# Optimization experiments

Hardware: AMD Instinct MI355X
Metric: run time of the kernel (lower is better)

Reference implementation:

```python
import jax, jax.numpy as jnp
import numpy as np
import math

DM, DP, P = 1024, 128, 256
B, S = 8, 4096

def setup_inputs() -> dict:
    key = jax.random.key(0)
    ks = jax.random.split(key, 7)
    sd = lambda fan_in: 1.0 / math.sqrt(fan_in)
    return {
        "x": jax.random.normal(ks[0], (B, S, DM), jnp.float32),
        "prim_embeds": jax.random.normal(ks[1], (P, DP), jnp.float32),
        "Wq": jax.random.normal(ks[2], (DP, DM), jnp.float32) * sd(DM),
        "Wk": jax.random.normal(ks[3], (DP, DP), jnp.float32) * sd(DP),
        "Wv": jax.random.normal(ks[4], (DP, DP), jnp.float32) * sd(DP),
        "Wo": jax.random.normal(ks[5], (DM, DP), jnp.float32) * sd(DP),
        "gate_w": jax.random.normal(ks[6], (1, DM), jnp.float32) * sd(DM),
        "gate_b": jnp.zeros((1,), jnp.float32),
    }

def reference(x, prim_embeds, Wq, Wk, Wv, Wo, gate_w, gate_b):
    # q: [B,S,dp]; k,v: [P,dp]
    q = jnp.einsum('bsm,pm->bsp', x, Wq)          # p here = d_prim
    k = prim_embeds @ Wk.T                         # [P, dp]
    v = prim_embeds @ Wv.T                         # [P, dp]
    scale = 1.0 / math.sqrt(q.shape[-1])
    scores = jnp.einsum('bsd,pd->bsp', q, k) * scale  # [B,S,P]
    attn = jax.nn.softmax(scores, axis=-1)
    ctx = jnp.einsum('bsp,pd->bsd', attn, v)       # [B,S,dp]
    out = jnp.einsum('bsd,md->bsm', ctx, Wo)       # [B,S,dm]
    gate = jax.nn.sigmoid(jnp.einsum('bsm,om->bso', x, gate_w) + gate_b)  # [B,S,1]
    return gate * out
```

## Files before the change

kernel.cpp:

```cpp
#include <hip/hip_runtime.h>
#include <hip/hip_bf16.h>

typedef unsigned short ushort_t;
typedef __attribute__((ext_vector_type(8))) short short8;
typedef __attribute__((ext_vector_type(8))) unsigned short ushort8;
typedef __attribute__((ext_vector_type(4))) float f32x4;

#define MFMA16(a,b,c) __builtin_amdgcn_mfma_f32_16x16x32_bf16((a),(b),(c),0,0,0)

__device__ __forceinline__ ushort_t f2bf(float f) {
  unsigned int u = __builtin_bit_cast(unsigned int, f);
  u += 0x7FFFu + ((u >> 16) & 1u);
  return (ushort_t)(u >> 16);
}
__device__ __forceinline__ unsigned int pack2bf(float a, float b) {
  unsigned int ua = __builtin_bit_cast(unsigned int, a);
  unsigned int ub = __builtin_bit_cast(unsigned int, b);
  ua += 0x7FFFu + ((ua >> 16) & 1u);
  ub += 0x7FFFu + ((ub >> 16) & 1u);
  return (ua >> 16) | (ub & 0xFFFF0000u);
}

#define DMd 1024
#define DPd 128
#define PPd 256

#define KWQ_OFF 0
#define KWQ_SIZE (8*17*4*512)
#define VWO_OFF KWQ_SIZE
#define VWO_SIZE (64*8*512)
#define KV_BYTE_OFF ((size_t)(KWQ_SIZE + VWO_SIZE) * 2)

__global__ __launch_bounds__(256) void prep1_kernel(
    const float* __restrict__ prim, const float* __restrict__ Wk,
    const float* __restrict__ Wv, ushort_t* __restrict__ ws) {
  __shared__ __align__(16) float Wl[128 * 132];
  __shared__ __align__(16) float pl[2 * 128];
  const int t = threadIdx.x;
  const int mat = blockIdx.x & 1;
  const int p0 = (blockIdx.x >> 1) * 2;
  const float* W = mat ? Wv : Wk;
  #pragma unroll
  for (int i = 0; i < 16; ++i) {
    int w = (i * 256 + t) * 4;
    int row = w >> 7, col = w & 127;
    *(float4*)&Wl[row * 132 + col] = *(const float4*)(W + w);
  }
  if (t < 64) {
    int row = t >> 5, col = (t & 31) * 4;
    *(float4*)&pl[row * 128 + col] = *(const float4*)(prim + (p0 + row) * 128 + col);
  }
  __syncthreads();
  const int d = t & 127, slot = t >> 7;
  float a0 = 0.f, a1 = 0.f, a2 = 0.f, a3 = 0.f;
  #pragma unroll
  for (int j = 0; j < 128; j += 4) {
    float4 w4 = *(const float4*)&Wl[d * 132 + j];
    float4 p4 = *(const float4*)&pl[slot * 128 + j];
    a0 += w4.x * p4.x; a1 += w4.y * p4.y; a2 += w4.z * p4.z; a3 += w4.w * p4.w;
  }
  float r = (a0 + a1) + (a2 + a3);
  float* kf = (float*)((char*)ws + KV_BYTE_OFF);
  float* vT = kf + 32768;
  if (mat == 0) kf[(p0 + slot) * 128 + d] = r;
  else          vT[d * 256 + p0 + slot] = r;
}

__global__ __launch_bounds__(256) void prep2_kernel(
    const float* __restrict__ Wq, const float* __restrict__ Wo,
    const float* __restrict__ gate_w, ushort_t* __restrict__ ws) {
  const float* kf = (const float*)((const char*)ws + KV_BYTE_OFF);
  const float* vT = kf + 32768;
  __shared__ __align__(16) float tile[8 * 128];
  const int b = blockIdx.x, t = threadIdx.x;
  float acc[8];
  #pragma unroll
  for (int j = 0; j < 8; ++j) acc[j] = 0.f;
  if (b < 136) {
    const int pt = b >> 2, ms = b & 3;
    const int p0 = pt * 8;
    const int p  = p0 + (t >> 5);
    const int m0 = ms * 256 + (t & 31) * 8;
    if (p0 < 256) {
      *(float4*)&tile[t * 4] = *(const float4*)(kf + p0 * 128 + t * 4);
      __syncthreads();
      const float* kp = &tile[(t >> 5) * 128];
      for (int d = 0; d < 128; d += 4) {
        float4 kv = *(const float4*)&kp[d];
        float4 qa0 = *(const float4*)(Wq + (d + 0) * 1024 + m0);
        float4 qb0 = *(const float4*)(Wq + (d + 0) * 1024 + m0 + 4);
        float4 qa1 = *(const float4*)(Wq + (d + 1) * 1024 + m0);
        float4 qb1 = *(const float4*)(Wq + (d + 1) * 1024 + m0 + 4);
        float4 qa2 = *(const float4*)(Wq + (d + 2) * 1024 + m0);
        float4 qb2 = *(const float4*)(Wq + (d + 2) * 1024 + m0 + 4);
        float4 qa3 = *(const float4*)(Wq + (d + 3) * 1024 + m0);
        float4 qb3 = *(const float4*)(Wq + (d + 3) * 1024 + m0 + 4);
        acc[0] += kv.x*qa0.x + kv.y*qa1.x + kv.z*qa2.x + kv.w*qa3.x;
        acc[1] += kv.x*qa0.y + kv.y*qa1.y + kv.z*qa2.y + kv.w*qa3.y;
        acc[2] += kv.x*qa0.z + kv.y*qa1.z + kv.z*qa2.z + kv.w*qa3.z;
        acc[3] += kv.x*qa0.w + kv.y*qa1.w + kv.z*qa2.w + kv.w*qa3.w;
        acc[4] += kv.x*qb0.x + kv.y*qb1.x + kv.z*qb2.x + kv.w*qb3.x;
        acc[5] += kv.x*qb0.y + kv.y*qb1.y + kv.z*qb2.y + kv.w*qb3.y;
        acc[6] += kv.x*qb0.z + kv.y*qb1.z + kv.z*qb2.z + kv.w*qb3.z;
        acc[7] += kv.x*qb0.w + kv.y*qb1.w + kv.z*qb2.w + kv.w*qb3.w;
      }
    } else if (p == 256) {
      #pragma unroll
      for (int j = 0; j < 8; ++j) acc[j] = gate_w[m0 + j];
    }
    const int c = m0 >> 7, ct = p >> 4, k4 = (m0 >> 5) & 3;
    const int row = ((m0 >> 3) & 3) * 16 + (p & 15);
    ushort8 u;
    #pragma unroll
    for (int j = 0; j < 8; ++j) u[j] = f2bf(acc[j]);
    *(ushort8*)&ws[KWQ_OFF + ((size_t)(c * 17 + ct) * 4 + k4) * 512 + (size_t)row * 8] = u;
  } else {
    const int mb  = b - 136;
    const int m0t = mb * 8;
    const int m   = m0t + (t >> 5);
    const int p8  = (t & 31) * 8;
    *(float4*)&tile[t * 4] = *(const float4*)(Wo + (size_t)m0t * 128 + t * 4);
    __syncthreads();
    const float* wo = &tile[(t >> 5) * 128];
    for (int d = 0; d < 128; d += 4) {
      float4 wv = *(const float4*)&wo[d];
      float4 va0 = *(const float4*)(vT + (d + 0) * 256 + p8);
      float4 vb0 = *(const float4*)(vT + (d + 0) * 256 + p8 + 4);
      float4 va1 = *(const float4*)(vT + (d + 1) * 256 + p8);
      float4 vb1 = *(const float4*)(vT + (d + 1) * 256 + p8 + 4);
      float4 va2 = *(const float4*)(vT + (d + 2) * 256 + p8);
      float4 vb2 = *(const float4*)(vT + (d + 2) * 256 + p8 + 4);
      float4 va3 = *(const float4*)(vT + (d + 3) * 256 + p8);
      float4 vb3 = *(const float4*)(vT + (d + 3) * 256 + p8 + 4);
      acc[0] += wv.x*va0.x + wv.y*va1.x + wv.z*va2.x + wv.w*va3.x;
      acc[1] += wv.x*va0.y + wv.y*va1.y + wv.z*va2.y + wv.w*va3.y;
      acc[2] += wv.x*va0.z + wv.y*va1.z + wv.z*va2.z + wv.w*va3.z;
      acc[3] += wv.x*va0.w + wv.y*va1.w + wv.z*va2.w + wv.w*va3.w;
      acc[4] += wv.x*vb0.x + wv.y*vb1.x + wv.z*vb2.x + wv.w*vb3.x;
      acc[5] += wv.x*vb0.y + wv.y*vb1.y + wv.z*vb2.y + wv.w*vb3.y;
      acc[6] += wv.x*vb0.z + wv.y*vb1.z + wv.z*vb2.z + wv.w*vb3.z;
      acc[7] += wv.x*vb0.w + wv.y*vb1.w + wv.z*vb2.w + wv.w*vb3.w;
    }
    const int ctg = m >> 4, k8 = p8 >> 5;
    const int row = ((p8 >> 3) & 3) * 16 + (m & 15);
    ushort8 u;
    #pragma unroll
    for (int j = 0; j < 8; ++j) u[j] = f2bf(acc[j]);
    *(ushort8*)&ws[VWO_OFF + ((size_t)(ctg * 8 + k8) * 512) + (size_t)row * 8] = u;
  }
}

#define LDX 136
#define LDSLAB 264

__global__ __launch_bounds__(256, 2) void fused_kernel(
    const float* __restrict__ x, const float* __restrict__ gate_b,
    const ushort_t* __restrict__ ws, float* __restrict__ out)
{
  __shared__ __align__(16) char smem[2 * 32 * LDX * 2 + 32 * 4 * 4 * 2 + 32 * 4];
  ushort_t* xt0      = (ushort_t*)smem;
  ushort_t* xt1      = xt0 + 32 * LDX;
  ushort_t* slab     = (ushort_t*)smem;
  float*    pmax     = (float*)(smem + 2 * 32 * LDX * 2);
  float*    psum     = pmax + 128;
  float*    gate_lds = psum + 128;

  const int t = threadIdx.x, wid = t >> 6, lane = t & 63;
  const int quad = lane >> 4, l16 = lane & 15;
  const int tok0 = blockIdx.x * 32;

  f32x4 acc[2][5];
  #pragma unroll
  for (int rt = 0; rt < 2; ++rt)
    #pragma unroll
    for (int ctl = 0; ctl < 5; ++ctl) acc[rt][ctl] = (f32x4){0.f,0.f,0.f,0.f};

  #pragma unroll
  for (int i = 0; i < 4; ++i) {
    int flat = i * 1024 + t * 4;
    int row = flat >> 7, col = flat & 127;
    float4 fv = *(const float4*)(x + (size_t)(tok0 + row) * 1024 + col);
    unsigned int pk0 = pack2bf(fv.x, fv.y), pk1 = pack2bf(fv.z, fv.w);
    *(unsigned long long*)&xt0[row * LDX + col] =
        (unsigned long long)pk0 | ((unsigned long long)pk1 << 32);
  }
  __syncthreads();

  for (int c = 0; c < 8; ++c) {
    ushort_t* cur = (c & 1) ? xt1 : xt0;
    ushort_t* nxt = (c & 1) ? xt0 : xt1;
    float4 fv[4];
    if (c < 7) {
      #pragma unroll
      for (int i = 0; i < 4; ++i) {
        int flat = i * 1024 + t * 4;
        int row = flat >> 7, col = flat & 127;
        fv[i] = *(const float4*)(x + (size_t)(tok0 + row) * 1024 + (c + 1) * 128 + col);
      }
    }
    #pragma unroll
    for (int k4 = 0; k4 < 4; ++k4) {
      short8 a[2];
      #pragma unroll
      for (int rt = 0; rt < 2; ++rt)
        a[rt] = *(const short8*)&cur[(rt * 16 + l16) * LDX + k4 * 32 + quad * 8];
      #pragma unroll
      for (int ctl = 0; ctl < 5; ++ctl) {
        if (ctl == 4 && wid != 3) continue;
        const int ct = wid * 4 + ctl;
        short8 bfr = *(const short8*)&ws[KWQ_OFF +
            ((size_t)(c * 17 + ct) * 4 + k4) * 512 + (size_t)lane * 8];
        #pragma unroll
        for (int rt = 0; rt < 2; ++rt) acc[rt][ctl] = MFMA16(a[rt], bfr, acc[rt][ctl]);
      }
    }
    if (c < 7) {
      #pragma unroll
      for (int i = 0; i < 4; ++i) {
        int flat = i * 1024 + t * 4;
        int row = flat >> 7, col = flat & 127;
        unsigned int pk0 = pack2bf(fv[i].x, fv[i].y), pk1 = pack2bf(fv[i].z, fv[i].w);
        *(unsigned long long*)&nxt[row * LDX + col] =
            (unsigned long long)pk0 | ((unsigned long long)pk1 << 32);
      }
      __syncthreads();
    }
  }

  const float SC = 0.08838834764831845f * 1.44269504088896f;
  float Mx[2][4];
  #pragma unroll
  for (int rt = 0; rt < 2; ++rt)
    #pragma unroll
    for (int r = 0; r < 4; ++r) {
      float m = acc[rt][0][r];
      #pragma unroll
      for (int ctl = 1; ctl < 4; ++ctl) m = fmaxf(m, acc[rt][ctl][r]);
      #pragma unroll
      for (int msk = 1; msk < 16; msk <<= 1) m = fmaxf(m, __shfl_xor(m, msk, 64));
      Mx[rt][r] = m;
    }
  if (l16 == 0) {
    #pragma unroll
    for (int rt = 0; rt < 2; ++rt)
      #pragma unroll
      for (int r = 0; r < 4; ++r)
        pmax[(rt * 16 + quad * 4 + r) * 4 + wid] = Mx[rt][r];
  }
  __syncthreads();
  float Mf[2][4];
  #pragma unroll
  for (int rt = 0; rt < 2; ++rt)
    #pragma unroll
    for (int r = 0; r < 4; ++r) {
      f32x4 pm = *(f32x4*)&pmax[(rt * 16 + quad * 4 + r) * 4];
      Mf[rt][r] = fmaxf(fmaxf(pm[0], pm[1]), fmaxf(pm[2], pm[3]));
    }
  float Sm[2][4];
  #pragma unroll
  for (int rt = 0; rt < 2; ++rt)
    #pragma unroll
    for (int r = 0; r < 4; ++r) Sm[rt][r] = 0.f;
  #pragma unroll
  for (int rt = 0; rt < 2; ++rt)
    #pragma unroll
    for (int ctl = 0; ctl < 4; ++ctl)
      #pragma unroll
      for (int r = 0; r < 4; ++r) {
        float e = exp2f((acc[rt][ctl][r] - Mf[rt][r]) * SC);
        acc[rt][ctl][r] = e;
        Sm[rt][r] += e;
      }
  #pragma unroll
  for (int rt = 0; rt < 2; ++rt)
    #pragma unroll
    for (int r = 0; r < 4; ++r) {
      #pragma unroll
      for (int msk = 1; msk < 16; msk <<= 1) Sm[rt][r] += __shfl_xor(Sm[rt][r], msk, 64);
    }
  if (l16 == 0) {
    #pragma unroll
    for (int rt = 0; rt < 2; ++rt)
      #pragma unroll
      for (int r = 0; r < 4; ++r)
        psum[(rt * 16 + quad * 4 + r) * 4 + wid] = Sm[rt][r];
    if (wid == 3) {
      float gb = gate_b[0];
      #pragma unroll
      for (int rt = 0; rt < 2; ++rt)
        #pragma unroll
        for (int r = 0; r < 4; ++r) {
          float lg = acc[rt][4][r] + gb;
          gate_lds[rt * 16 + quad * 4 + r] = 1.f / (1.f + __expf(-lg));
        }
    }
  }
  __syncthreads();
  float scl[2][4];
  #pragma unroll
  for (int rt = 0; rt < 2; ++rt)
    #pragma unroll
    for (int r = 0; r < 4; ++r) {
      f32x4 ps = *(f32x4*)&psum[(rt * 16 + quad * 4 + r) * 4];
      float g = gate_lds[rt * 16 + quad * 4 + r];
      scl[rt][r] = g / (ps[0] + ps[1] + ps[2] + ps[3]);
    }

  #pragma unroll
  for (int rt = 0; rt < 2; ++rt)
    #pragma unroll
    for (int ctl = 0; ctl < 4; ++ctl)
      #pragma unroll
      for (int r = 0; r < 4; ++r)
        slab[(rt * 16 + quad * 4 + r) * LDSLAB + (wid * 4 + ctl) * 16 + l16] =
            f2bf(acc[rt][ctl][r] * scl[rt][r]);
  __syncthreads();

  short8 af[2][8];
  #pragma unroll
  for (int rt = 0; rt < 2; ++rt)
    #pragma unroll
    for (int k8 = 0; k8 < 8; ++k8)
      af[rt][k8] = *(const short8*)&slab[(rt * 16 + l16) * LDSLAB + k8 * 32 + quad * 8];

  const int n0 = wid * 256;
  const ushort_t* vb = ws + VWO_OFF + (size_t)(n0 >> 4) * (8 * 512) + (size_t)lane * 8;

  short8 bfA[8], bfB[8];
  #pragma unroll
  for (int k8 = 0; k8 < 8; ++k8)
    bfA[k8] = *(const short8*)&vb[(size_t)k8 * 512];

  #pragma unroll 2
  for (int ntp = 0; ntp < 8; ++ntp) {
    const int ntA = ntp * 2, ntB = ntA + 1;
    #pragma unroll
    for (int k8 = 0; k8 < 8; ++k8)
      bfB[k8] = *(const short8*)&vb[(size_t)(ntB * 8 + k8) * 512];
    {
      f32x4 oa[2];
      #pragma unroll
      for (int rt = 0; rt < 2; ++rt) oa[rt] = (f32x4){0.f,0.f,0.f,0.f};
      #pragma unroll
      for (int rt = 0; rt < 2; ++rt)
        #pragma unroll
        for (int k8 = 0; k8 < 8; ++k8)
          oa[rt] = MFMA16(af[rt][k8], bfA[k8], oa[rt]);
      #pragma unroll
      for (int rt = 0; rt < 2; ++rt)
        #pragma unroll
        for (int r = 0; r < 4; ++r)
          __builtin_nontemporal_store(oa[rt][r],
              &out[(size_t)(tok0 + rt * 16 + quad * 4 + r) * 1024 + n0 + ntA * 16 + l16]);
    }
    if (ntp < 7) {
      #pragma unroll
      for (int k8 = 0; k8 < 8; ++k8)
        bfA[k8] = *(const short8*)&vb[(size_t)((ntA + 2) * 8 + k8) * 512];
    }
    {
      f32x4 oa[2];
      #pragma unroll
      for (int rt = 0; rt < 2; ++rt) oa[rt] = (f32x4){0.f,0.f,0.f,0.f};
      #pragma unroll
      for (int rt = 0; rt < 2; ++rt)
        #pragma unroll
        for (int k8 = 0; k8 < 8; ++k8)
          oa[rt] = MFMA16(af[rt][k8], bfB[k8], oa[rt]);
      #pragma unroll
      for (int rt = 0; rt < 2; ++rt)
        #pragma unroll
        for (int r = 0; r < 4; ++r)
          __builtin_nontemporal_store(oa[rt][r],
              &out[(size_t)(tok0 + rt * 16 + quad * 4 + r) * 1024 + n0 + ntB * 16 + l16]);
    }
  }
}

extern "C" void kernel_launch(void* const* d_in, const int* in_sizes, int n_in,
                              void* d_out, int out_size, void* d_ws, size_t ws_size,
                              hipStream_t stream) {
  const float* x    = (const float*)d_in[0];
  const float* prim = (const float*)d_in[1];
  const float* Wq   = (const float*)d_in[2];
  const float* Wk   = (const float*)d_in[3];
  const float* Wv   = (const float*)d_in[4];
  const float* Wo   = (const float*)d_in[5];
  const float* gw   = (const float*)d_in[6];
  const float* gb   = (const float*)d_in[7];
  float* out = (float*)d_out;
  ushort_t* ws = (ushort_t*)d_ws;

  prep1_kernel<<<256, 256, 0, stream>>>(prim, Wk, Wv, ws);
  prep2_kernel<<<264, 256, 0, stream>>>(Wq, Wo, gw, ws);
  fused_kernel<<<1024, 256, 0, stream>>>(x, gb, ws, out);
}
```

Measured before the change: 348.9 us.

## Enlarge fused block to 64 tokens with 8 waves and register-pipelined weight loads

Result: slower. 393.0 us (+12.6%).

```diff
diff --git a/kernel.cpp b/kernel.cpp
--- a/kernel.cpp
+++ b/kernel.cpp
@@ -153,32 +153,36 @@
 #define LDX 136
 #define LDSLAB 264
 
-__global__ __launch_bounds__(256, 2) void fused_kernel(
+__global__ __launch_bounds__(512, 4) void fused_kernel(
     const float* __restrict__ x, const float* __restrict__ gate_b,
     const ushort_t* __restrict__ ws, float* __restrict__ out)
 {
-  __shared__ __align__(16) char smem[2 * 32 * LDX * 2 + 32 * 4 * 4 * 2 + 32 * 4];
+  __shared__ __align__(16) char smem[2 * 64 * LDX * 2 + 64 * 8 * 4 * 2 + 64 * 4];
   ushort_t* xt0      = (ushort_t*)smem;
-  ushort_t* xt1      = xt0 + 32 * LDX;
+  ushort_t* xt1      = xt0 + 64 * LDX;
   ushort_t* slab     = (ushort_t*)smem;
-  float*    pmax     = (float*)(smem + 2 * 32 * LDX * 2);
-  float*    psum     = pmax + 128;
-  float*    gate_lds = psum + 128;
+  float*    pmax     = (float*)(smem + 2 * 64 * LDX * 2);
+  float*    psum     = pmax + 64 * 8;
+  float*    gate_lds = psum + 64 * 8;
 
   const int t = threadIdx.x, wid = t >> 6, lane = t & 63;
   const int quad = lane >> 4, l16 = lane & 15;
-  const int tok0 = blockIdx.x * 32;
-
-  f32x4 acc[2][5];
-  #pragma unroll
-  for (int rt = 0; rt < 2; ++rt)
-    #pragma unroll
-    for (int ctl = 0; ctl < 5; ++ctl) acc[rt][ctl] = (f32x4){0.f,0.f,0.f,0.f};
+  const int tok0 = blockIdx.x * 64;
+  const int ct0 = wid * 2;
+  const bool gw7 = (wid == 7);
+
+  f32x4 acc[4][2];
+  f32x4 accG[4];
+  #pragma unroll
+  for (int rt = 0; rt < 4; ++rt) {
+    acc[rt][0] = (f32x4){0.f,0.f,0.f,0.f};
+    acc[rt][1] = (f32x4){0.f,0.f,0.f,0.f};
+    accG[rt]   = (f32x4){0.f,0.f,0.f,0.f};
+  }
 
   #pragma unroll
   for (int i = 0; i < 4; ++i) {
-    int flat = i * 1024 + t * 4;
-    int row = flat >> 7, col = flat & 127;
+    int row = i * 16 + (t >> 5), col = (t & 31) * 4;
     float4 fv = *(const float4*)(x + (size_t)(tok0 + row) * 1024 + col);
     unsigned int pk0 = pack2bf(fv.x, fv.y), pk1 = pack2bf(fv.z, fv.w);
     *(unsigned long long*)&xt0[row * LDX + col] =
@@ -193,32 +197,48 @@
     if (c < 7) {
       #pragma unroll
       for (int i = 0; i < 4; ++i) {
-        int flat = i * 1024 + t * 4;
-        int row = flat >> 7, col = flat & 127;
+        int row = i * 16 + (t >> 5), col = (t & 31) * 4;
         fv[i] = *(const float4*)(x + (size_t)(tok0 + row) * 1024 + (c + 1) * 128 + col);
       }
     }
+    const ushort_t* wb = ws + KWQ_OFF + (size_t)(c * 17) * 4 * 512 + (size_t)lane * 8;
+    short8 b0[2], b1[2], g0, g1;
+    b0[0] = *(const short8*)&wb[(size_t)((ct0 + 0) * 4 + 0) * 512];
+    b0[1] = *(const short8*)&wb[(size_t)((ct0 + 1) * 4 + 0) * 512];
+    if (gw7) g0 = *(const short8*)&wb[(size_t)(16 * 4 + 0) * 512];
     #pragma unroll
     for (int k4 = 0; k4 < 4; ++k4) {
-      short8 a[2];
-      #pragma unroll
-      for (int rt = 0; rt < 2; ++rt)
+      short8 a[4];
+      #pragma unroll
+      for (int rt = 0; rt < 4; ++rt)
         a[rt] = *(const short8*)&cur[(rt * 16 + l16) * LDX + k4 * 32 + quad * 8];
-      #pragma unroll
-      for (int ctl = 0; ctl < 5; ++ctl) {
-        if (ctl == 4 && wid != 3) continue;
-        const int ct = wid * 4 + ctl;
-        short8 bfr = *(const short8*)&ws[KWQ_OFF +
-            ((size_t)(c * 17 + ct) * 4 + k4) * 512 + (size_t)lane * 8];
+      if (k4 < 3) {
+        if (k4 & 1) {
+          b0[0] = *(const short8*)&wb[(size_t)((ct0 + 0) * 4 + k4 + 1) * 512];
+          b0[1] = *(const short8*)&wb[(size_t)((ct0 + 1) * 4 + k4 + 1) * 512];
+          if (gw7) g0 = *(const short8*)&wb[(size_t)(16 * 4 + k4 + 1) * 512];
+        } else {
+          b1[0] = *(const short8*)&wb[(size_t)((ct0 + 0) * 4 + k4 + 1) * 512];
+          b1[1] = *(const short8*)&wb[(size_t)((ct0 + 1) * 4 + k4 + 1) * 512];
+          if (gw7) g1 = *(const short8*)&wb[(size_t)(16 * 4 + k4 + 1) * 512];
+        }
+      }
+      const short8* bc = (k4 & 1) ? b1 : b0;
+      const short8  gc = (k4 & 1) ? g1 : g0;
+      #pragma unroll
+      for (int rt = 0; rt < 4; ++rt) {
+        acc[rt][0] = MFMA16(a[rt], bc[0], acc[rt][0]);
+        acc[rt][1] = MFMA16(a[rt], bc[1], acc[rt][1]);
+      }
+      if (gw7) {
         #pragma unroll
-        for (int rt = 0; rt < 2; ++rt) acc[rt][ctl] = MFMA16(a[rt], bfr, acc[rt][ctl]);
+        for (int rt = 0; rt < 4; ++rt) accG[rt] = MFMA16(a[rt], gc, accG[rt]);
       }
     }
     if (c < 7) {
       #pragma unroll
       for (int i = 0; i < 4; ++i) {
-        int flat = i * 1024 + t * 4;
-        int row = flat >> 7, col = flat & 127;
+        int row = i * 16 + (t >> 5), col = (t & 31) * 4;
         unsigned int pk0 = pack2bf(fv[i].x, fv[i].y), pk1 = pack2bf(fv[i].z, fv[i].w);
         *(unsigned long long*)&nxt[row * LDX + col] =
             (unsigned long long)pk0 | ((unsigned long long)pk1 << 32);
@@ -228,151 +248,117 @@
   }
 
   const float SC = 0.08838834764831845f * 1.44269504088896f;
-  float Mx[2][4];
-  #pragma unroll
-  for (int rt = 0; rt < 2; ++rt)
-    #pragma unroll
-    for (int r = 0; r < 4; ++r) {
-      float m = acc[rt][0][r];
-      #pragma unroll
-      for (int ctl = 1; ctl < 4; ++ctl) m = fmaxf(m, acc[rt][ctl][r]);
+  float Mx[4];
+  #pragma unroll
+  for (int rt = 0; rt < 4; ++rt)
+    #pragma unroll
+    for (int r = 0; r < 4; ++r) {
+      float m = fmaxf(acc[rt][0][r], acc[rt][1][r]);
       #pragma unroll
       for (int msk = 1; msk < 16; msk <<= 1) m = fmaxf(m, __shfl_xor(m, msk, 64));
-      Mx[rt][r] = m;
+      if (r == 0) Mx[rt] = m;
+      if (l16 == 0) pmax[(rt * 16 + quad * 4 + r) * 8 + wid] = m;
+    }
+  (void)Mx;
+  __syncthreads();
+  float Mf[4][4];
+  #pragma unroll
+  for (int rt = 0; rt < 4; ++rt)
+    #pragma unroll
+    for (int r = 0; r < 4; ++r) {
+      f32x4 p0v = *(f32x4*)&pmax[(rt * 16 + quad * 4 + r) * 8];
+      f32x4 p1v = *(f32x4*)&pmax[(rt * 16 + quad * 4 + r) * 8 + 4];
+      Mf[rt][r] = fmaxf(fmaxf(fmaxf(p0v[0], p0v[1]), fmaxf(p0v[2], p0v[3])),
+                        fmaxf(fmaxf(p1v[0], p1v[1]), fmaxf(p1v[2], p1v[3])));
+    }
+  float Sm[4][4];
+  #pragma unroll
+  for (int rt = 0; rt < 4; ++rt)
+    #pragma unroll
+    for (int r = 0; r < 4; ++r) {
+      float e0 = exp2f((acc[rt][0][r] - Mf[rt][r]) * SC);
+      float e1 = exp2f((acc[rt][1][r] - Mf[rt][r]) * SC);
+      acc[rt][0][r] = e0; acc[rt][1][r] = e1;
+      Sm[rt][r] = e0 + e1;
+    }
+  #pragma unroll
+  for (int rt = 0; rt < 4; ++rt)
+    #pragma unroll
+    for (int r = 0; r < 4; ++r) {
+      #pragma unroll
+      for (int msk = 1; msk < 16; msk <<= 1) Sm[rt][r] += __shfl_xor(Sm[rt][r], msk, 64);
     }
   if (l16 == 0) {
     #pragma unroll
-    for (int rt = 0; rt < 2; ++rt)
+    for (int rt = 0; rt < 4; ++rt)
       #pragma unroll
       for (int r = 0; r < 4; ++r)
-        pmax[(rt * 16 + quad * 4 + r) * 4 + wid] = Mx[rt][r];
-  }
-  __syncthreads();
-  float Mf[2][4];
-  #pragma unroll
-  for (int rt = 0; rt < 2; ++rt)
-    #pragma unroll
-    for (int r = 0; r < 4; ++r) {
-      f32x4 pm = *(f32x4*)&pmax[(rt * 16 + quad * 4 + r) * 4];
-      Mf[rt][r] = fmaxf(fmaxf(pm[0], pm[1]), fmaxf(pm[2], pm[3]));
-    }
-  float Sm[2][4];
-  #pragma unroll
-  for (int rt = 0; rt < 2; ++rt)
-    #pragma unroll
-    for (int r = 0; r < 4; ++r) Sm[rt][r] = 0.f;
-  #pragma unroll
-  for (int rt = 0; rt < 2; ++rt)
-    #pragma unroll
-    for (int ctl = 0; ctl < 4; ++ctl)
-      #pragma unroll
-      for (int r = 0; r < 4; ++r) {
-        float e = exp2f((acc[rt][ctl][r] - Mf[rt][r]) * SC);
-        acc[rt][ctl][r] = e;
-        Sm[rt][r] += e;
-      }
-  #pragma unroll
-  for (int rt = 0; rt < 2; ++rt)
-    #pragma unroll
-    for (int r = 0; r < 4; ++r) {
-      #pragma unroll
-      for (int msk = 1; msk < 16; msk <<= 1) Sm[rt][r] += __shfl_xor(Sm[rt][r], msk, 64);
-    }
-  if (l16 == 0) {
-    #pragma unroll
-    for (int rt = 0; rt < 2; ++rt)
-      #pragma unroll
-      for (int r = 0; r < 4; ++r)
-        psum[(rt * 16 + quad * 4 + r) * 4 + wid] = Sm[rt][r];
-    if (wid == 3) {
+        psum[(rt * 16 + quad * 4 + r) * 8 + wid] = Sm[rt][r];
+    if (gw7) {
       float gb = gate_b[0];
       #pragma unroll
-      for (int rt = 0; rt < 2; ++rt)
+      for (int rt = 0; rt < 4; ++rt)
         #pragma unroll
         for (int r = 0; r < 4; ++r) {
-          float lg = acc[rt][4][r] + gb;
+          float lg = accG[rt][r] + gb;
           gate_lds[rt * 16 + quad * 4 + r] = 1.f / (1.f + __expf(-lg));
         }
     }
   }
   __syncthreads();
-  float scl[2][4];
-  #pragma unroll
-  for (int rt = 0; rt < 2; ++rt)
-    #pragma unroll
-    for (int r = 0; r < 4; ++r) {
-      f32x4 ps = *(f32x4*)&psum[(rt * 16 + quad * 4 + r) * 4];
-      float g = gate_lds[rt * 16 + quad * 4 + r];
-      scl[rt][r] = g / (ps[0] + ps[1] + ps[2] + ps[3]);
-    }
-
-  #pragma unroll
-  for (int rt = 0; rt < 2; ++rt)
-    #pragma unroll
-    for (int ctl = 0; ctl < 4; ++ctl)
+  float scl[4][4];
+  #pragma unroll
+  for (int rt = 0; rt < 4; ++rt)
+    #pragma unroll
+    for (int r = 0; r < 4; ++r) {
+      int row = rt * 16 + quad * 4 + r;
+      f32x4 s0v = *(f32x4*)&psum[row * 8];
+      f32x4 s1v = *(f32x4*)&psum[row * 8 + 4];
+      float s = (s0v[0] + s0v[1] + s0v[2] + s0v[3]) + (s1v[0] + s1v[1] + s1v[2] + s1v[3]);
+      scl[rt][r] = gate_lds[row] / s;
+    }
+
+  #pragma unroll
+  for (int rt = 0; rt < 4; ++rt)
+    #pragma unroll
+    for (int ctl = 0; ctl < 2; ++ctl)
       #pragma unroll
       for (int r = 0; r < 4; ++r)
-        slab[(rt * 16 + quad * 4 + r) * LDSLAB + (wid * 4 + ctl) * 16 + l16] =
+        slab[(rt * 16 + quad * 4 + r) * LDSLAB + (ct0 + ctl) * 16 + l16] =
             f2bf(acc[rt][ctl][r] * scl[rt][r]);
   __syncthreads();
 
-  short8 af[2][8];
-  #pragma unroll
-  for (int rt = 0; rt < 2; ++rt)
-    #pragma unroll
-    for (int k8 = 0; k8 < 8; ++k8)
-      af[rt][k8] = *(const short8*)&slab[(rt * 16 + l16) * LDSLAB + k8 * 32 + quad * 8];
-
-  const int n0 = wid * 256;
-  const ushort_t* vb = ws + VWO_OFF + (size_t)(n0 >> 4) * (8 * 512) + (size_t)lane * 8;
+  const int n0 = wid * 128;
+  const ushort_t* vb = ws + VWO_OFF + (size_t)(wid * 8) * (8 * 512) + (size_t)lane * 8;
 
   short8 bfA[8], bfB[8];
   #pragma unroll
   for (int k8 = 0; k8 < 8; ++k8)
     bfA[k8] = *(const short8*)&vb[(size_t)k8 * 512];
 
-  #pragma unroll 2
-  for (int ntp = 0; ntp < 8; ++ntp) {
-    const int ntA = ntp * 2, ntB = ntA + 1;
-    #pragma unroll
-    for (int k8 = 0; k8 < 8; ++k8)
-      bfB[k8] = *(const short8*)&vb[(size_t)(ntB * 8 + k8) * 512];
-    {
-      f32x4 oa[2];
-      #pragma unroll
-      for (int rt = 0; rt < 2; ++rt) oa[rt] = (f32x4){0.f,0.f,0.f,0.f};
-      #pragma unroll
-      for (int rt = 0; rt < 2; ++rt)
-        #pragma unroll
-        for (int k8 = 0; k8 < 8; ++k8)
-          oa[rt] = MFMA16(af[rt][k8], bfA[k8], oa[rt]);
-      #pragma unroll
-      for (int rt = 0; rt < 2; ++rt)
-        #pragma unroll
-        for (int r = 0; r < 4; ++r)
-          __builtin_nontemporal_store(oa[rt][r],
-              &out[(size_t)(tok0 + rt * 16 + quad * 4 + r) * 1024 + n0 + ntA * 16 + l16]);
-    }
-    if (ntp < 7) {
+  #pragma unroll
+  for (int nt = 0; nt < 8; ++nt) {
+    if (nt < 7) {
+      short8* bfn = (nt & 1) ? bfA : bfB;
       #pragma unroll
       for (int k8 = 0; k8 < 8; ++k8)
-        bfA[k8] = *(const short8*)&vb[(size_t)((ntA + 2) * 8 + k8) * 512];
-    }
-    {
-      f32x4 oa[2];
-      #pragma unroll
-      for (int rt = 0; rt < 2; ++rt) oa[rt] = (f32x4){0.f,0.f,0.f,0.f};
-      #pragma unroll
-      for (int rt = 0; rt < 2; ++rt)
-        #pragma unroll
-        for (int k8 = 0; k8 < 8; ++k8)
-          oa[rt] = MFMA16(af[rt][k8], bfB[k8], oa[rt]);
-      #pragma unroll
-      for (int rt = 0; rt < 2; ++rt)
-        #pragma unroll
-        for (int r = 0; r < 4; ++r)
-          __builtin_nontemporal_store(oa[rt][r],
-              &out[(size_t)(tok0 + rt * 16 + quad * 4 + r) * 1024 + n0 + ntB * 16 + l16]);
+        bfn[k8] = *(const short8*)&vb[(size_t)((nt + 1) * 8 + k8) * 512];
+    }
+    const short8* bfc = (nt & 1) ? bfB : bfA;
+    #pragma unroll
+    for (int rt = 0; rt < 4; ++rt) {
+      short8 af8[8];
+      #pragma unroll
+      for (int k8 = 0; k8 < 8; ++k8)
+        af8[k8] = *(const short8*)&slab[(rt * 16 + l16) * LDSLAB + k8 * 32 + quad * 8];
+      f32x4 oa = (f32x4){0.f,0.f,0.f,0.f};
+      #pragma unroll
+      for (int k8 = 0; k8 < 8; ++k8)
+        oa = MFMA16(af8[k8], bfc[k8], oa);
+      #pragma unroll
+      for (int r = 0; r < 4; ++r)
+        __builtin_nontemporal_store(oa[r],
+            &out[(size_t)(tok0 + rt * 16 + quad * 4 + r) * 1024 + n0 + nt * 16 + l16]);
     }
   }
 }
@@ -393,5 +379,5 @@
 
   prep1_kernel<<<256, 256, 0, stream>>>(prim, Wk, Wv, ws);
   prep2_kernel<<<264, 256, 0, stream>>>(Wq, Wo, gw, ws);
-  fused_kernel<<<1024, 256, 0, stream>>>(x, gb, ws, out);
-}
+  fused_kernel<<<512, 512, 0, stream>>>(x, gb, ws, out);
+}
```

## Load x directly into MFMA fragments from global, drop LDS staging

Applied to the files above, without the earlier changes.

Result: slower. 405.6 us (+16.2%).

```diff
diff --git a/kernel.cpp b/kernel.cpp
--- a/kernel.cpp
+++ b/kernel.cpp
@@ -5,6 +5,7 @@
 typedef __attribute__((ext_vector_type(8))) short short8;
 typedef __attribute__((ext_vector_type(8))) unsigned short ushort8;
 typedef __attribute__((ext_vector_type(4))) float f32x4;
+typedef __attribute__((ext_vector_type(4))) unsigned int u32x4;
 
 #define MFMA16(a,b,c) __builtin_amdgcn_mfma_f32_16x16x32_bf16((a),(b),(c),0,0,0)
 
@@ -19,6 +20,12 @@
   ua += 0x7FFFu + ((ua >> 16) & 1u);
   ub += 0x7FFFu + ((ub >> 16) & 1u);
   return (ua >> 16) | (ub & 0xFFFF0000u);
+}
+__device__ __forceinline__ short8 pack8(float4 lo, float4 hi) {
+  u32x4 u;
+  u.x = pack2bf(lo.x, lo.y); u.y = pack2bf(lo.z, lo.w);
+  u.z = pack2bf(hi.x, hi.y); u.w = pack2bf(hi.z, hi.w);
+  return __builtin_bit_cast(short8, u);
 }
 
 #define DMd 1024
@@ -150,24 +157,22 @@
   }
 }
 
-#define LDX 136
 #define LDSLAB 264
 
-__global__ __launch_bounds__(256, 2) void fused_kernel(
+__global__ __launch_bounds__(256, 4) void fused_kernel(
     const float* __restrict__ x, const float* __restrict__ gate_b,
     const ushort_t* __restrict__ ws, float* __restrict__ out)
 {
-  __shared__ __align__(16) char smem[2 * 32 * LDX * 2 + 32 * 4 * 4 * 2 + 32 * 4];
-  ushort_t* xt0      = (ushort_t*)smem;
-  ushort_t* xt1      = xt0 + 32 * LDX;
+  __shared__ __align__(16) char smem[32 * LDSLAB * 2 + 32 * 4 * 4 * 2 + 32 * 4];
   ushort_t* slab     = (ushort_t*)smem;
-  float*    pmax     = (float*)(smem + 2 * 32 * LDX * 2);
+  float*    pmax     = (float*)(smem + 32 * LDSLAB * 2);
   float*    psum     = pmax + 128;
   float*    gate_lds = psum + 128;
 
   const int t = threadIdx.x, wid = t >> 6, lane = t & 63;
   const int quad = lane >> 4, l16 = lane & 15;
   const int tok0 = blockIdx.x * 32;
+  const int ct0 = wid * 4;
 
   f32x4 acc[2][5];
   #pragma unroll
@@ -175,60 +180,39 @@
     #pragma unroll
     for (int ctl = 0; ctl < 5; ++ctl) acc[rt][ctl] = (f32x4){0.f,0.f,0.f,0.f};
 
-  #pragma unroll
-  for (int i = 0; i < 4; ++i) {
-    int flat = i * 1024 + t * 4;
-    int row = flat >> 7, col = flat & 127;
-    float4 fv = *(const float4*)(x + (size_t)(tok0 + row) * 1024 + col);
-    unsigned int pk0 = pack2bf(fv.x, fv.y), pk1 = pack2bf(fv.z, fv.w);
-    *(unsigned long long*)&xt0[row * LDX + col] =
-        (unsigned long long)pk0 | ((unsigned long long)pk1 << 32);
-  }
-  __syncthreads();
-
+  const float* xr0 = x + (size_t)(tok0 + l16) * 1024 + quad * 8;
+  const float* xr1 = xr0 + 16 * 1024;
   for (int c = 0; c < 8; ++c) {
-    ushort_t* cur = (c & 1) ? xt1 : xt0;
-    ushort_t* nxt = (c & 1) ? xt0 : xt1;
-    float4 fv[4];
-    if (c < 7) {
-      #pragma unroll
-      for (int i = 0; i < 4; ++i) {
-        int flat = i * 1024 + t * 4;
-        int row = flat >> 7, col = flat & 127;
-        fv[i] = *(const float4*)(x + (size_t)(tok0 + row) * 1024 + (c + 1) * 128 + col);
-      }
-    }
+    const ushort_t* wb = ws + KWQ_OFF + (size_t)(c * 17) * 4 * 512 + (size_t)lane * 8;
+    const float* px0 = xr0 + c * 128;
+    const float* px1 = xr1 + c * 128;
     #pragma unroll
     for (int k4 = 0; k4 < 4; ++k4) {
-      short8 a[2];
-      #pragma unroll
-      for (int rt = 0; rt < 2; ++rt)
-        a[rt] = *(const short8*)&cur[(rt * 16 + l16) * LDX + k4 * 32 + quad * 8];
-      #pragma unroll
-      for (int ctl = 0; ctl < 5; ++ctl) {
-        if (ctl == 4 && wid != 3) continue;
-        const int ct = wid * 4 + ctl;
-        short8 bfr = *(const short8*)&ws[KWQ_OFF +
-            ((size_t)(c * 17 + ct) * 4 + k4) * 512 + (size_t)lane * 8];
-        #pragma unroll
-        for (int rt = 0; rt < 2; ++rt) acc[rt][ctl] = MFMA16(a[rt], bfr, acc[rt][ctl]);
-      }
-    }
-    if (c < 7) {
-      #pragma unroll
-      for (int i = 0; i < 4; ++i) {
-        int flat = i * 1024 + t * 4;
-        int row = flat >> 7, col = flat & 127;
-        unsigned int pk0 = pack2bf(fv[i].x, fv[i].y), pk1 = pack2bf(fv[i].z, fv[i].w);
-        *(unsigned long long*)&nxt[row * LDX + col] =
-            (unsigned long long)pk0 | ((unsigned long long)pk1 << 32);
-      }
-      __syncthreads();
+      float4 fa0 = *(const float4*)(px0 + k4 * 32);
+      float4 fa1 = *(const float4*)(px0 + k4 * 32 + 4);
+      float4 fb0 = *(const float4*)(px1 + k4 * 32);
+      float4 fb1 = *(const float4*)(px1 + k4 * 32 + 4);
+      short8 b0 = *(const short8*)&wb[(size_t)((ct0 + 0) * 4 + k4) * 512];
+      short8 b1 = *(const short8*)&wb[(size_t)((ct0 + 1) * 4 + k4) * 512];
+      short8 b2 = *(const short8*)&wb[(size_t)((ct0 + 2) * 4 + k4) * 512];
+      short8 b3 = *(const short8*)&wb[(size_t)((ct0 + 3) * 4 + k4) * 512];
+      short8 b4 = *(const short8*)&wb[(size_t)((ct0 + 4) * 4 + k4) * 512];
+      short8 a0 = pack8(fa0, fa1);
+      short8 a1 = pack8(fb0, fb1);
+      acc[0][0] = MFMA16(a0, b0, acc[0][0]);
+      acc[1][0] = MFMA16(a1, b0, acc[1][0]);
+      acc[0][1] = MFMA16(a0, b1, acc[0][1]);
+      acc[1][1] = MFMA16(a1, b1, acc[1][1]);
+      acc[0][2] = MFMA16(a0, b2, acc[0][2]);
+      acc[1][2] = MFMA16(a1, b2, acc[1][2]);
+      acc[0][3] = MFMA16(a0, b3, acc[0][3]);
+      acc[1][3] = MFMA16(a1, b3, acc[1][3]);
+      acc[0][4] = MFMA16(a0, b4, acc[0][4]);
+      acc[1][4] = MFMA16(a1, b4, acc[1][4]);
     }
   }
 
   const float SC = 0.08838834764831845f * 1.44269504088896f;
-  float Mx[2][4];
   #pragma unroll
   for (int rt = 0; rt < 2; ++rt)
     #pragma unroll
@@ -238,15 +222,8 @@
       for (int ctl = 1; ctl < 4; ++ctl) m = fmaxf(m, acc[rt][ctl][r]);
       #pragma unroll
       for (int msk = 1; msk < 16; msk <<= 1) m = fmaxf(m, __shfl_xor(m, msk, 64));
-      Mx[rt][r] = m;
-    }
-  if (l16 == 0) {
-    #pragma unroll
-    for (int rt = 0; rt < 2; ++rt)
-      #pragma unroll
-      for (int r = 0; r < 4; ++r)
-        pmax[(rt * 16 + quad * 4 + r) * 4 + wid] = Mx[rt][r];
-  }
+      if (l16 == 0) pmax[(rt * 16 + quad * 4 + r) * 4 + wid] = m;
+    }
   __syncthreads();
   float Mf[2][4];
   #pragma unroll
@@ -312,7 +289,7 @@
     for (int ctl = 0; ctl < 4; ++ctl)
       #pragma unroll
       for (int r = 0; r < 4; ++r)
-        slab[(rt * 16 + quad * 4 + r) * LDSLAB + (wid * 4 + ctl) * 16 + l16] =
+        slab[(rt * 16 + quad * 4 + r) * LDSLAB + (ct0 + ctl) * 16 + l16] =
             f2bf(acc[rt][ctl][r] * scl[rt][r]);
   __syncthreads();
 
```

## Raise occupancy target and drop double-buffered Wo fragment prefetch in output GEMM

Applied to the files above, without the earlier changes.

New measurement: 520.7 us. +49.2%, slower.

```diff
diff --git a/kernel.cpp b/kernel.cpp
--- a/kernel.cpp
+++ b/kernel.cpp
@@ -153,7 +153,7 @@
 #define LDX 136
 #define LDSLAB 264
 
-__global__ __launch_bounds__(256, 2) void fused_kernel(
+__global__ __launch_bounds__(256, 8) void fused_kernel(
     const float* __restrict__ x, const float* __restrict__ gate_b,
     const ushort_t* __restrict__ ws, float* __restrict__ out)
 {
@@ -228,7 +228,6 @@
   }
 
   const float SC = 0.08838834764831845f * 1.44269504088896f;
-  float Mx[2][4];
   #pragma unroll
   for (int rt = 0; rt < 2; ++rt)
     #pragma unroll
@@ -238,15 +237,8 @@
       for (int ctl = 1; ctl < 4; ++ctl) m = fmaxf(m, acc[rt][ctl][r]);
       #pragma unroll
       for (int msk = 1; msk < 16; msk <<= 1) m = fmaxf(m, __shfl_xor(m, msk, 64));
-      Mx[rt][r] = m;
-    }
-  if (l16 == 0) {
-    #pragma unroll
-    for (int rt = 0; rt < 2; ++rt)
-      #pragma unroll
-      for (int r = 0; r < 4; ++r)
-        pmax[(rt * 16 + quad * 4 + r) * 4 + wid] = Mx[rt][r];
-  }
+      if (l16 == 0) pmax[(rt * 16 + quad * 4 + r) * 4 + wid] = m;
+    }
   __syncthreads();
   float Mf[2][4];
   #pragma unroll
@@ -324,56 +316,26 @@
       af[rt][k8] = *(const short8*)&slab[(rt * 16 + l16) * LDSLAB + k8 * 32 + quad * 8];
 
   const int n0 = wid * 256;
-  const ushort_t* vb = ws + VWO_OFF + (size_t)(n0 >> 4) * (8 * 512) + (size_t)lane * 8;
-
-  short8 bfA[8], bfB[8];
-  #pragma unroll
-  for (int k8 = 0; k8 < 8; ++k8)
-    bfA[k8] = *(const short8*)&vb[(size_t)k8 * 512];
-
-  #pragma unroll 2
-  for (int ntp = 0; ntp < 8; ++ntp) {
-    const int ntA = ntp * 2, ntB = ntA + 1;
+  for (int nt = 0; nt < 16; ++nt) {
+    const int ctg = (n0 >> 4) + nt;
+    short8 bf[8];
     #pragma unroll
     for (int k8 = 0; k8 < 8; ++k8)
-      bfB[k8] = *(const short8*)&vb[(size_t)(ntB * 8 + k8) * 512];
-    {
-      f32x4 oa[2];
-      #pragma unroll
-      for (int rt = 0; rt < 2; ++rt) oa[rt] = (f32x4){0.f,0.f,0.f,0.f};
-      #pragma unroll
-      for (int rt = 0; rt < 2; ++rt)
-        #pragma unroll
-        for (int k8 = 0; k8 < 8; ++k8)
-          oa[rt] = MFMA16(af[rt][k8], bfA[k8], oa[rt]);
-      #pragma unroll
-      for (int rt = 0; rt < 2; ++rt)
-        #pragma unroll
-        for (int r = 0; r < 4; ++r)
-          __builtin_nontemporal_store(oa[rt][r],
-              &out[(size_t)(tok0 + rt * 16 + quad * 4 + r) * 1024 + n0 + ntA * 16 + l16]);
-    }
-    if (ntp < 7) {
+      bf[k8] = *(const short8*)&ws[VWO_OFF + ((size_t)(ctg * 8 + k8) * 512) + (size_t)lane * 8];
+    f32x4 oa[2];
+    #pragma unroll
+    for (int rt = 0; rt < 2; ++rt) oa[rt] = (f32x4){0.f,0.f,0.f,0.f};
+    #pragma unroll
+    for (int rt = 0; rt < 2; ++rt)
       #pragma unroll
       for (int k8 = 0; k8 < 8; ++k8)
-        bfA[k8] = *(const short8*)&vb[(size_t)((ntA + 2) * 8 + k8) * 512];
-    }
-    {
-      f32x4 oa[2];
-      #pragma unroll
-      for (int rt = 0; rt < 2; ++rt) oa[rt] = (f32x4){0.f,0.f,0.f,0.f};
-      #pragma unroll
-      for (int rt = 0; rt < 2; ++rt)
-        #pragma unroll
-        for (int k8 = 0; k8 < 8; ++k8)
-          oa[rt] = MFMA16(af[rt][k8], bfB[k8], oa[rt]);
-      #pragma unroll
-      for (int rt = 0; rt < 2; ++rt)
-        #pragma unroll
-        for (int r = 0; r < 4; ++r)
-          __builtin_nontemporal_store(oa[rt][r],
-              &out[(size_t)(tok0 + rt * 16 + quad * 4 + r) * 1024 + n0 + ntB * 16 + l16]);
-    }
+        oa[rt] = MFMA16(af[rt][k8], bf[k8], oa[rt]);
+    #pragma unroll
+    for (int rt = 0; rt < 2; ++rt)
+      #pragma unroll
+      for (int r = 0; r < 4; ++r)
+        __builtin_nontemporal_store(oa[rt][r],
+            &out[(size_t)(tok0 + rt * 16 + quad * 4 + r) * 1024 + n0 + nt * 16 + l16]);
   }
 }
 
```
